# Optimization experiments

Hardware: AMD Instinct MI355X
Metric: run time of the kernel (lower is better)

Reference implementation:

```python
import jax, jax.numpy as jnp
import numpy as np

# SofthebbArgs constants (rate, adaptive=True, p, dot_uw=False, temp)
RATE = 1e-3
TEMP = 1.0
P = 0.5


def negate_non_maximal(t):
    # keep the per-row max entry, negate all others
    idx = jnp.argmax(t, axis=-1)                      # [B]
    mask = idx[:, None] == jnp.arange(t.shape[-1])    # [B, OUT]
    return jnp.where(mask, t, -t)


def setup_inputs() -> dict:
    key = jax.random.key(0)
    k1, k2 = jax.random.split(key, 2)
    B, IN, OUT = 8192, 1024, 1024
    x = jax.random.normal(k1, (B, IN), dtype=jnp.float32)
    # xavier_normal_ with gain=1: std = sqrt(2/(fan_in+fan_out))
    W = jax.random.normal(k2, (OUT, IN), dtype=jnp.float32) * (2.0 / (IN + OUT)) ** 0.5
    b = jnp.zeros((OUT,), dtype=jnp.float32)
    return {"x": x, "W": W, "b": b}


def reference(x, W, b):
    # --- HebbianLinear.forward (act = Identity) ---
    u = x @ W.T + b                                   # [B, OUT]
    y = u
    # --- softhebb: y = softmax(y / temp), then _hebb with dot_uw=False ---
    ysm = jax.nn.softmax(y / TEMP, axis=1)
    yn = negate_non_maximal(ysm)                      # [B, OUT]
    Bn = x.shape[0]
    # _hebb materializes dw[b,o,i] = yn[b,o]*(x[b,i] - u[b,o]*W[o,i]) then means over b.
    # Algebraically fused (no [B,OUT,IN] intermediate):
    #   step[o,i] = (yn^T x)[o,i]/B - mean_b(yn[b,o]*u[b,o]) * W[o,i]
    step = (yn.T @ x) / Bn - jnp.mean(yn * u, axis=0)[:, None] * W  # [OUT, IN]
    # adaptive per-row rate: rate * |1 - ||W_row||_2|^p
    diff = jnp.abs(1.0 - jnp.linalg.norm(W, axis=1))  # [OUT]
    rate = RATE * diff ** P
    return rate[:, None] * step                       # [OUT, IN]
```

## Files before the change

kernel.cpp:

```cpp
#include <hip/hip_runtime.h>

#define BATCH 8192
#define INF_  1024
#define OUTF  1024
#define INV_B (1.0f/8192.0f)
#define RATE_C 1e-3f
#define SPLITZ 16

typedef __bf16 bf16x8 __attribute__((ext_vector_type(8)));
typedef float  f32x4  __attribute__((ext_vector_type(4)));
typedef const __attribute__((address_space(1))) unsigned int* gas_t;
typedef __attribute__((address_space(3))) unsigned int* las_t;

static __device__ __forceinline__ unsigned short f2bf(float f) {
  unsigned int u = __float_as_uint(f);
  u += 0x7fffu + ((u >> 16) & 1u);
  return (unsigned short)(u >> 16);
}
static __device__ __forceinline__ float bf2f(unsigned short h) {
  return __uint_as_float(((unsigned int)h) << 16);
}

__global__ __launch_bounds__(256) void k_convert(
    const float* __restrict__ x, unsigned short* __restrict__ xb,
    unsigned short* __restrict__ xT, const float* __restrict__ W,
    unsigned short* __restrict__ Wb, float* __restrict__ rate) {
  const int t = threadIdx.x;
  if (blockIdx.x >= 2048) {
    __shared__ float red[256];
    const int o = blockIdx.x - 2048;
    float4 v = *(const float4*)&W[(size_t)o * INF_ + t * 4];
    ushort4 h;
    h.x = f2bf(v.x); h.y = f2bf(v.y); h.z = f2bf(v.z); h.w = f2bf(v.w);
    *(ushort4*)&Wb[(size_t)o * INF_ + t * 4] = h;
    red[t] = v.x * v.x + v.y * v.y + v.z * v.z + v.w * v.w;
    __syncthreads();
    for (int s = 128; s > 0; s >>= 1) {
      if (t < s) red[t] += red[t + s];
      __syncthreads();
    }
    if (t == 0) {
      float nrm = sqrtf(red[0]);
      rate[o] = RATE_C * sqrtf(fabsf(1.0f - nrm));
    }
    return;
  }
  __shared__ unsigned int t32[64][33];
  const int bx = blockIdx.x & 15;
  const int by = blockIdx.x >> 4;
  const int r0 = by * 64;
  const int c0 = bx * 64;
  const int m = t & 15;
  const int q = t >> 4;
#pragma unroll
  for (int p = 0; p < 2; ++p) {
    const int r2 = p * 16 + q;
    const int b  = r0 + 2 * r2;
    float4 v0 = *(const float4*)&x[(size_t)b * INF_ + c0 + 4 * m];
    float4 v1 = *(const float4*)&x[(size_t)(b + 1) * INF_ + c0 + 4 * m];
    ushort4 h0, h1;
    h0.x = f2bf(v0.x); h0.y = f2bf(v0.y); h0.z = f2bf(v0.z); h0.w = f2bf(v0.w);
    h1.x = f2bf(v1.x); h1.y = f2bf(v1.y); h1.z = f2bf(v1.z); h1.w = f2bf(v1.w);
    *(ushort4*)&xb[(size_t)b * INF_ + c0 + 4 * m] = h0;
    *(ushort4*)&xb[(size_t)(b + 1) * INF_ + c0 + 4 * m] = h1;
    t32[4 * m + 0][r2] = (unsigned int)h0.x | ((unsigned int)h1.x << 16);
    t32[4 * m + 1][r2] = (unsigned int)h0.y | ((unsigned int)h1.y << 16);
    t32[4 * m + 2][r2] = (unsigned int)h0.z | ((unsigned int)h1.z << 16);
    t32[4 * m + 3][r2] = (unsigned int)h0.w | ((unsigned int)h1.w << 16);
  }
  __syncthreads();
  const int c  = t >> 2;
  const int sg = t & 3;
  unsigned int vb[8];
#pragma unroll
  for (int k = 0; k < 8; ++k) vb[k] = t32[c][sg * 8 + k];
  unsigned short* dst = &xT[(size_t)(c0 + c) * BATCH + r0 + sg * 16];
  *(uint4*)&dst[0] = make_uint4(vb[0], vb[1], vb[2], vb[3]);
  *(uint4*)&dst[8] = make_uint4(vb[4], vb[5], vb[6], vb[7]);
}

__global__ __launch_bounds__(256, 3) void k_gemm(
    const unsigned short* __restrict__ A, const unsigned short* __restrict__ B,
    int lda, int ldb, int kChunk, float* __restrict__ C, int ldc,
    const float* __restrict__ bias, int mode) {
  __shared__ unsigned short As[128 * 64];
  __shared__ unsigned short Bs[128 * 64];
  const int t  = threadIdx.x;
  const int id = blockIdx.x;
  int bx, by, bz;
  if (mode == 0) {
    by = (id & 7) | ((id >> 6) << 3);
    bx = (id >> 3) & 7;
    bz = 0;
  } else {
    bz = ((id & 7) << 1) | ((id >> 3) & 1);
    by = (id >> 4) & 7;
    bx = id >> 7;
  }
  const int m0   = by * 128;
  const int n0   = bx * 128;
  const int k0   = bz * kChunk;
  const int lane = t & 63;
  const int wave = t >> 6;
  const int sr   = lane >> 3;
  const int scx  = ((lane & 7) ^ sr) * 8;
  const int wm   = (wave >> 1) * 64;
  const int wn   = (wave & 1) * 64;
  const int fm   = lane & 15;
  const int fk   = (lane >> 4) * 8;

  f32x4 acc[4][4] = {};

  const int ldsRow0 = wave * 8;
  const size_t gArow = (size_t)(m0 + ldsRow0 + sr) * lda + scx;
  const size_t gBrow = (size_t)(n0 + ldsRow0 + sr) * ldb + scx;

  for (int ks = 0; ks < kChunk; ks += 64) {
    const int k = k0 + ks;
#pragma unroll
    for (int j = 0; j < 4; ++j) {
      __builtin_amdgcn_global_load_lds(
          (gas_t)&A[gArow + (size_t)j * 32 * lda + k],
          (las_t)&As[(ldsRow0 + j * 32) * 64], 16, 0, 0);
      __builtin_amdgcn_global_load_lds(
          (gas_t)&B[gBrow + (size_t)j * 32 * ldb + k],
          (las_t)&Bs[(ldsRow0 + j * 32) * 64], 16, 0, 0);
    }
    __syncthreads();
#pragma unroll
    for (int kk = 0; kk < 64; kk += 32) {
      bf16x8 af[4], bf[4];
      const int swz = ((((kk + fk) >> 3) ^ (fm & 7)) << 3);
#pragma unroll
      for (int i = 0; i < 4; ++i)
        af[i] = *(const bf16x8*)&As[(wm + i * 16 + fm) * 64 + swz];
#pragma unroll
      for (int i = 0; i < 4; ++i)
        bf[i] = *(const bf16x8*)&Bs[(wn + i * 16 + fm) * 64 + swz];
#pragma unroll
      for (int mt = 0; mt < 4; ++mt)
#pragma unroll
        for (int nt = 0; nt < 4; ++nt)
          acc[mt][nt] = __builtin_amdgcn_mfma_f32_16x16x32_bf16(
              af[mt], bf[nt], acc[mt][nt], 0, 0, 0);
    }
    __syncthreads();
  }

  const int er = (lane >> 4) * 4;
  if (mode == 0) {
#pragma unroll
    for (int nt = 0; nt < 4; ++nt) {
      const int n  = n0 + wn + nt * 16 + fm;
      const float bv = bias[n];
#pragma unroll
      for (int mt = 0; mt < 4; ++mt) {
        const int mb = m0 + wm + mt * 16 + er;
#pragma unroll
        for (int r = 0; r < 4; ++r)
          C[(size_t)(mb + r) * ldc + n] = acc[mt][nt][r] + bv;
      }
    }
  } else {
    unsigned short* Cp = (unsigned short*)C + (size_t)bz * (1024u * 1024u);
#pragma unroll
    for (int nt = 0; nt < 4; ++nt) {
      const int n = n0 + wn + nt * 16 + fm;
#pragma unroll
      for (int mt = 0; mt < 4; ++mt) {
        const int mb = m0 + wm + mt * 16 + er;
#pragma unroll
        for (int r = 0; r < 4; ++r)
          Cp[(size_t)(mb + r) * ldc + n] = f2bf(acc[mt][nt][r]);
      }
    }
  }
}

__global__ __launch_bounds__(256) void k_row_stats(
    const float* __restrict__ u, const float* __restrict__ x,
    const float* __restrict__ W, float* __restrict__ rowmax,
    float* __restrict__ rowinv, int* __restrict__ rowarg) {
  __shared__ int cands[4][32];
  __shared__ int cnt[4];
  const int lane = threadIdx.x & 63;
  const int wave = threadIdx.x >> 6;
  const int b    = blockIdx.x * 4 + wave;

  float a[16];
  const float* up = &u[(size_t)b * OUTF + lane * 16];
#pragma unroll
  for (int j = 0; j < 16; j += 4) {
    float4 v = *(const float4*)&up[j];
    a[j] = v.x; a[j + 1] = v.y; a[j + 2] = v.z; a[j + 3] = v.w;
  }
  float mv = a[0]; int mi = lane * 16;
#pragma unroll
  for (int j = 1; j < 16; ++j)
    if (a[j] > mv) { mv = a[j]; mi = lane * 16 + j; }
#pragma unroll
  for (int off = 1; off < 64; off <<= 1) {
    float ov = __shfl_xor(mv, off);
    int   oi = __shfl_xor(mi, off);
    if (ov > mv || (ov == mv && oi < mi)) { mv = ov; mi = oi; }
  }
  const float M = mv;
  float se = 0.0f;
#pragma unroll
  for (int j = 0; j < 16; ++j) se += __expf(a[j] - M);
#pragma unroll
  for (int off = 1; off < 64; off <<= 1) se += __shfl_xor(se, off);

  const float thr = M - 0.05f;
  int ccount = 0;
  unsigned int cflags = 0;
#pragma unroll
  for (int j = 0; j < 16; ++j)
    if (a[j] >= thr) { cflags |= (1u << j); ++ccount; }
  int tot = ccount;
#pragma unroll
  for (int off = 1; off < 64; off <<= 1) tot += __shfl_xor(tot, off);

  int best = mi;
  if (tot > 1) {
    if (lane == 0) cnt[wave] = 0;
    for (int j = 0; j < 16; ++j)
      if (cflags & (1u << j)) {
        int p = atomicAdd(&cnt[wave], 1);
        if (p < 32) cands[wave][p] = lane * 16 + j;
      }
    int nc = cnt[wave]; if (nc > 32) nc = 32;
    float xr[16];
    const float* xp = &x[(size_t)b * INF_ + lane * 16];
#pragma unroll
    for (int j = 0; j < 16; j += 4) {
      float4 v = *(const float4*)&xp[j];
      xr[j] = v.x; xr[j + 1] = v.y; xr[j + 2] = v.z; xr[j + 3] = v.w;
    }
    float bv = -3.4e38f; int bi = 0x7fffffff;
    for (int c = 0; c < nc; ++c) {
      const int o = cands[wave][c];
      const float* wp = &W[(size_t)o * INF_ + lane * 16];
      float d = 0.0f;
#pragma unroll
      for (int j = 0; j < 16; j += 4) {
        float4 v = *(const float4*)&wp[j];
        d += xr[j] * v.x + xr[j + 1] * v.y + xr[j + 2] * v.z + xr[j + 3] * v.w;
      }
#pragma unroll
      for (int off = 1; off < 64; off <<= 1) d += __shfl_xor(d, off);
      if (d > bv || (d == bv && o < bi)) { bv = d; bi = o; }
    }
    best = bi;
  }
  if (lane == 0) {
    rowmax[b] = M;
    rowinv[b] = 1.0f / se;
    rowarg[b] = best;
  }
}

__global__ __launch_bounds__(256) void k_yn(
    const float* __restrict__ u, const float* __restrict__ rowmax,
    const float* __restrict__ rowinv, const int* __restrict__ rowarg,
    unsigned short* __restrict__ ynT, float* __restrict__ s_part) {
  __shared__ unsigned short tile[256][72];
  __shared__ float smax[64], sinv[64];
  __shared__ int   sarg[64];
  const int t  = threadIdx.x;
  const int o0 = blockIdx.x * 256;
  const int b0 = blockIdx.y * 64;
  if (t < 64) {
    smax[t] = rowmax[b0 + t];
    sinv[t] = rowinv[b0 + t];
    sarg[t] = rowarg[b0 + t];
  }
  __syncthreads();
  const int o = o0 + t;
  float sacc = 0.0f;
#pragma unroll
  for (int g = 0; g < 8; ++g) {
    uint4 pkv;
    unsigned short* pk = (unsigned short*)&pkv;
#pragma unroll
    for (int j = 0; j < 8; ++j) {
      const int r = g * 8 + j;
      float uu  = u[(size_t)(b0 + r) * OUTF + o];
      float ysm = __expf(uu - smax[r]) * sinv[r];
      float yn  = (o == sarg[r]) ? ysm : -ysm;
      sacc += yn * uu;
      pk[j] = f2bf(yn);
    }
    *(uint4*)&tile[t][g * 8] = pkv;
  }
  s_part[(size_t)blockIdx.y * OUTF + o] = sacc;
  __syncthreads();
#pragma unroll
  for (int it = 0; it < 8; ++it) {
    const int row = it * 32 + (t >> 3);
    const int seg = (t & 7) * 8;
    uint4 vv = *(const uint4*)&tile[row][seg];
    *(uint4*)&ynT[(size_t)(o0 + row) * BATCH + b0 + seg] = vv;
  }
}

__global__ __launch_bounds__(256) void k_final(
    const unsigned short* __restrict__ Cp, const float* __restrict__ W,
    const float* __restrict__ s_part, const float* __restrict__ rate,
    float* __restrict__ out) {
  __shared__ float sred[128];
  const int t = threadIdx.x;
  const int o = blockIdx.x;
  if (t < 128) sred[t] = s_part[(size_t)t * OUTF + o];
  __syncthreads();
  for (int s2 = 64; s2 > 0; s2 >>= 1) {
    if (t < s2) sred[t] += sred[t + s2];
    __syncthreads();
  }
  const float sb = sred[0] * INV_B;
  const float rt = rate[o];
  const int i0 = t * 4;
  float cx = 0, cy = 0, cz = 0, cw = 0;
#pragma unroll
  for (int z = 0; z < SPLITZ; ++z) {
    ushort4 h = *(const ushort4*)&Cp[(size_t)z * (1024u * 1024u) +
                                     (size_t)o * INF_ + i0];
    cx += bf2f(h.x); cy += bf2f(h.y); cz += bf2f(h.z); cw += bf2f(h.w);
  }
  float4 w = *(const float4*)&W[(size_t)o * INF_ + i0];
  float4 r;
  r.x = rt * (cx * INV_B - sb * w.x);
  r.y = rt * (cy * INV_B - sb * w.y);
  r.z = rt * (cz * INV_B - sb * w.z);
  r.w = rt * (cw * INV_B - sb * w.w);
  *(float4*)&out[(size_t)o * INF_ + i0] = r;
}

extern "C" void kernel_launch(void* const* d_in, const int* in_sizes, int n_in,
                              void* d_out, int out_size, void* d_ws, size_t ws_size,
                              hipStream_t stream) {
  const float* x    = (const float*)d_in[0];
  const float* W    = (const float*)d_in[1];
  const float* bias = (const float*)d_in[2];
  float* out = (float*)d_out;
  char* ws = (char*)d_ws;

  float*          u     = (float*)(ws + 0);
  unsigned short* xb    = (unsigned short*)(ws + 33554432);
  unsigned short* xT    = (unsigned short*)(ws + 50331648);
  unsigned short* Wb    = (unsigned short*)(ws + 67108864);
  unsigned short* ynT   = (unsigned short*)(ws + 69206016);
  float*          rate  = (float*)(ws + 85983232);
  float*          rmax  = (float*)(ws + 85987328);
  float*          rinv  = (float*)(ws + 86020096);
  int*            rarg  = (int*)  (ws + 86052864);
  float*          spart = (float*)(ws + 86085632);

  k_convert<<<dim3(3072), 256, 0, stream>>>(x, xb, xT, W, Wb, rate);
  k_gemm<<<dim3(512), 256, 0, stream>>>(xb, Wb, 1024, 1024, 1024,
                                        u, 1024, bias, 0);
  k_row_stats<<<dim3(2048), 256, 0, stream>>>(u, x, W, rmax, rinv, rarg);
  k_yn<<<dim3(4, 128), 256, 0, stream>>>(u, rmax, rinv, rarg, ynT, spart);
  k_gemm<<<dim3(1024), 256, 0, stream>>>(ynT, xT, 8192, 8192, 512,
                                         u, 1024, nullptr, 1);
  k_final<<<dim3(1024), 256, 0, stream>>>((const unsigned short*)u, W, spart,
                                          rate, out);
}
```

Measured before the change: 156.9 us.

## Store logits as bf16 and fuse row stats with yn transpose kernel

The first GEMM now writes u as bf16 instead of fp32, halving the logit traffic. Row max, softmax sum, argmax tie-breaking, yn computation, the s partial sums and the transposed ynT store are fused into one kernel that processes 16 rows per block through a swizzled LDS tile. This removes one launch and the extra pass over u. In exchange, bf16 logits coarsen the softmax and argmax inputs (the candidate threshold is widened to compensate), and k_final must reduce 2048 partial rows instead of 128.

```diff
diff --git a/kernel.cpp b/kernel.cpp
--- a/kernel.cpp
+++ b/kernel.cpp
@@ -81,7 +81,7 @@
 
 __global__ __launch_bounds__(256, 3) void k_gemm(
     const unsigned short* __restrict__ A, const unsigned short* __restrict__ B,
-    int lda, int ldb, int kChunk, float* __restrict__ C, int ldc,
+    int lda, int ldb, int kChunk, void* __restrict__ C, int ldc,
     const float* __restrict__ bias, int mode) {
   __shared__ unsigned short As[128 * 64];
   __shared__ unsigned short Bs[128 * 64];
@@ -149,6 +149,7 @@
 
   const int er = (lane >> 4) * 4;
   if (mode == 0) {
+    unsigned short* Cb = (unsigned short*)C;
 #pragma unroll
     for (int nt = 0; nt < 4; ++nt) {
       const int n  = n0 + wn + nt * 16 + fm;
@@ -158,7 +159,7 @@
         const int mb = m0 + wm + mt * 16 + er;
 #pragma unroll
         for (int r = 0; r < 4; ++r)
-          C[(size_t)(mb + r) * ldc + n] = acc[mt][nt][r] + bv;
+          Cb[(size_t)(mb + r) * ldc + n] = f2bf(acc[mt][nt][r] + bv);
       }
     }
   } else {
@@ -177,130 +178,145 @@
   }
 }
 
-__global__ __launch_bounds__(256) void k_row_stats(
-    const float* __restrict__ u, const float* __restrict__ x,
-    const float* __restrict__ W, float* __restrict__ rowmax,
-    float* __restrict__ rowinv, int* __restrict__ rowarg) {
+__global__ __launch_bounds__(256, 2) void k_softhebb(
+    const unsigned short* __restrict__ ub, const float* __restrict__ x,
+    const float* __restrict__ W, unsigned short* __restrict__ ynT,
+    float* __restrict__ s_part) {
+  __shared__ unsigned short tile[16][1032];
   __shared__ int cands[4][32];
   __shared__ int cnt[4];
-  const int lane = threadIdx.x & 63;
-  const int wave = threadIdx.x >> 6;
-  const int b    = blockIdx.x * 4 + wave;
-
-  float a[16];
-  const float* up = &u[(size_t)b * OUTF + lane * 16];
-#pragma unroll
-  for (int j = 0; j < 16; j += 4) {
-    float4 v = *(const float4*)&up[j];
-    a[j] = v.x; a[j + 1] = v.y; a[j + 2] = v.z; a[j + 3] = v.w;
-  }
-  float mv = a[0]; int mi = lane * 16;
-#pragma unroll
-  for (int j = 1; j < 16; ++j)
-    if (a[j] > mv) { mv = a[j]; mi = lane * 16 + j; }
-#pragma unroll
-  for (int off = 1; off < 64; off <<= 1) {
-    float ov = __shfl_xor(mv, off);
-    int   oi = __shfl_xor(mi, off);
-    if (ov > mv || (ov == mv && oi < mi)) { mv = ov; mi = oi; }
-  }
-  const float M = mv;
-  float se = 0.0f;
-#pragma unroll
-  for (int j = 0; j < 16; ++j) se += __expf(a[j] - M);
-#pragma unroll
-  for (int off = 1; off < 64; off <<= 1) se += __shfl_xor(se, off);
-
-  const float thr = M - 0.05f;
-  int ccount = 0;
-  unsigned int cflags = 0;
-#pragma unroll
-  for (int j = 0; j < 16; ++j)
-    if (a[j] >= thr) { cflags |= (1u << j); ++ccount; }
-  int tot = ccount;
-#pragma unroll
-  for (int off = 1; off < 64; off <<= 1) tot += __shfl_xor(tot, off);
-
-  int best = mi;
-  if (tot > 1) {
-    if (lane == 0) cnt[wave] = 0;
+  const int t     = threadIdx.x;
+  const int lane  = t & 63;
+  const int wave  = t >> 6;
+  const int b0    = blockIdx.x * 16;
+  const int oBase = lane * 16;
+
+  float sacc[16];
+#pragma unroll
+  for (int j = 0; j < 16; ++j) sacc[j] = 0.0f;
+
+  for (int rw = 0; rw < 4; ++rw) {
+    const int r = wave * 4 + rw;
+    const int b = b0 + r;
+    float a[16];
+    {
+      uint4 q0 = *(const uint4*)&ub[(size_t)b * OUTF + oBase];
+      uint4 q1 = *(const uint4*)&ub[(size_t)b * OUTF + oBase + 8];
+      const unsigned int* qa = (const unsigned int*)&q0;
+      const unsigned int* qb = (const unsigned int*)&q1;
+#pragma unroll
+      for (int c = 0; c < 4; ++c) {
+        a[2 * c]     = __uint_as_float(qa[c] << 16);
+        a[2 * c + 1] = __uint_as_float(qa[c] & 0xffff0000u);
+        a[8 + 2 * c]     = __uint_as_float(qb[c] << 16);
+        a[8 + 2 * c + 1] = __uint_as_float(qb[c] & 0xffff0000u);
+      }
+    }
+    float mv = a[0]; int mi = oBase;
+#pragma unroll
+    for (int j = 1; j < 16; ++j)
+      if (a[j] > mv) { mv = a[j]; mi = oBase + j; }
+#pragma unroll
+    for (int off = 1; off < 64; off <<= 1) {
+      float ov = __shfl_xor(mv, off);
+      int   oi = __shfl_xor(mi, off);
+      if (ov > mv || (ov == mv && oi < mi)) { mv = ov; mi = oi; }
+    }
+    const float M = mv;
+    float se = 0.0f;
+#pragma unroll
+    for (int j = 0; j < 16; ++j) se += __expf(a[j] - M);
+#pragma unroll
+    for (int off = 1; off < 64; off <<= 1) se += __shfl_xor(se, off);
+
+    const float thr = M - 0.10f;
+    unsigned int cflags = 0;
+    int ccount = 0;
+#pragma unroll
     for (int j = 0; j < 16; ++j)
-      if (cflags & (1u << j)) {
-        int p = atomicAdd(&cnt[wave], 1);
-        if (p < 32) cands[wave][p] = lane * 16 + j;
-      }
-    int nc = cnt[wave]; if (nc > 32) nc = 32;
-    float xr[16];
-    const float* xp = &x[(size_t)b * INF_ + lane * 16];
-#pragma unroll
-    for (int j = 0; j < 16; j += 4) {
-      float4 v = *(const float4*)&xp[j];
-      xr[j] = v.x; xr[j + 1] = v.y; xr[j + 2] = v.z; xr[j + 3] = v.w;
-    }
-    float bv = -3.4e38f; int bi = 0x7fffffff;
-    for (int c = 0; c < nc; ++c) {
-      const int o = cands[wave][c];
-      const float* wp = &W[(size_t)o * INF_ + lane * 16];
-      float d = 0.0f;
+      if (a[j] >= thr) { cflags |= (1u << j); ++ccount; }
+    int tot = ccount;
+#pragma unroll
+    for (int off = 1; off < 64; off <<= 1) tot += __shfl_xor(tot, off);
+
+    int best = mi;
+    if (tot > 1) {
+      if (lane == 0) cnt[wave] = 0;
+      for (int j = 0; j < 16; ++j)
+        if (cflags & (1u << j)) {
+          int p = atomicAdd(&cnt[wave], 1);
+          if (p < 32) cands[wave][p] = oBase + j;
+        }
+      int nc = cnt[wave]; if (nc > 32) nc = 32;
+      float xr[16];
+      const float* xp = &x[(size_t)b * INF_ + oBase];
 #pragma unroll
       for (int j = 0; j < 16; j += 4) {
-        float4 v = *(const float4*)&wp[j];
-        d += xr[j] * v.x + xr[j + 1] * v.y + xr[j + 2] * v.z + xr[j + 3] * v.w;
-      }
-#pragma unroll
-      for (int off = 1; off < 64; off <<= 1) d += __shfl_xor(d, off);
-      if (d > bv || (d == bv && o < bi)) { bv = d; bi = o; }
-    }
-    best = bi;
-  }
-  if (lane == 0) {
-    rowmax[b] = M;
-    rowinv[b] = 1.0f / se;
-    rowarg[b] = best;
-  }
-}
-
-__global__ __launch_bounds__(256) void k_yn(
-    const float* __restrict__ u, const float* __restrict__ rowmax,
-    const float* __restrict__ rowinv, const int* __restrict__ rowarg,
-    unsigned short* __restrict__ ynT, float* __restrict__ s_part) {
-  __shared__ unsigned short tile[256][72];
-  __shared__ float smax[64], sinv[64];
-  __shared__ int   sarg[64];
-  const int t  = threadIdx.x;
-  const int o0 = blockIdx.x * 256;
-  const int b0 = blockIdx.y * 64;
-  if (t < 64) {
-    smax[t] = rowmax[b0 + t];
-    sinv[t] = rowinv[b0 + t];
-    sarg[t] = rowarg[b0 + t];
+        float4 v = *(const float4*)&xp[j];
+        xr[j] = v.x; xr[j + 1] = v.y; xr[j + 2] = v.z; xr[j + 3] = v.w;
+      }
+      float bv = -3.4e38f; int bi = 0x7fffffff;
+      for (int c = 0; c < nc; ++c) {
+        const int o = cands[wave][c];
+        const float* wp = &W[(size_t)o * INF_ + oBase];
+        float d = 0.0f;
+#pragma unroll
+        for (int j = 0; j < 16; j += 4) {
+          float4 v = *(const float4*)&wp[j];
+          d += xr[j] * v.x + xr[j + 1] * v.y + xr[j + 2] * v.z +
+               xr[j + 3] * v.w;
+        }
+#pragma unroll
+        for (int off = 1; off < 64; off <<= 1) d += __shfl_xor(d, off);
+        if (d > bv || (d == bv && o < bi)) { bv = d; bi = o; }
+      }
+      best = bi;
+    }
+
+    const float inv = 1.0f / se;
+    uint4 pka, pkb;
+    unsigned short* p0v = (unsigned short*)&pka;
+    unsigned short* p1v = (unsigned short*)&pkb;
+#pragma unroll
+    for (int j = 0; j < 16; ++j) {
+      float e  = __expf(a[j] - M) * inv;
+      float yn = (oBase + j == best) ? e : -e;
+      sacc[j] += yn * a[j];
+      unsigned short hv = f2bf(yn);
+      if (j < 8) p0v[j] = hv; else p1v[j - 8] = hv;
+    }
+    const int c0 = 2 * lane, c1 = 2 * lane + 1;
+    const int sp0 = c0 ^ ((c0 >> 1) & 7);
+    const int sp1 = c1 ^ ((c1 >> 1) & 7);
+    *(uint4*)&tile[r][sp0 * 8] = pka;
+    *(uint4*)&tile[r][sp1 * 8] = pkb;
+  }
+
+  {
+    float* sp = &s_part[(size_t)(blockIdx.x * 4 + wave) * OUTF + oBase];
+#pragma unroll
+    for (int j = 0; j < 16; j += 4)
+      *(float4*)&sp[j] = make_float4(sacc[j], sacc[j + 1], sacc[j + 2],
+                                     sacc[j + 3]);
   }
   __syncthreads();
-  const int o = o0 + t;
-  float sacc = 0.0f;
-#pragma unroll
-  for (int g = 0; g < 8; ++g) {
-    uint4 pkv;
-    unsigned short* pk = (unsigned short*)&pkv;
-#pragma unroll
-    for (int j = 0; j < 8; ++j) {
-      const int r = g * 8 + j;
-      float uu  = u[(size_t)(b0 + r) * OUTF + o];
-      float ysm = __expf(uu - smax[r]) * sinv[r];
-      float yn  = (o == sarg[r]) ? ysm : -ysm;
-      sacc += yn * uu;
-      pk[j] = f2bf(yn);
-    }
-    *(uint4*)&tile[t][g * 8] = pkv;
-  }
-  s_part[(size_t)blockIdx.y * OUTF + o] = sacc;
-  __syncthreads();
-#pragma unroll
-  for (int it = 0; it < 8; ++it) {
-    const int row = it * 32 + (t >> 3);
-    const int seg = (t & 7) * 8;
-    uint4 vv = *(const uint4*)&tile[row][seg];
-    *(uint4*)&ynT[(size_t)(o0 + row) * BATCH + b0 + seg] = vv;
+
+#pragma unroll
+  for (int i = 0; i < 4; ++i) {
+    const int o  = t + 256 * i;
+    const int c  = o >> 3;
+    const int sp = c ^ ((c >> 1) & 7);
+    const int off = o & 7;
+    uint4 v0, v1;
+    unsigned short* va = (unsigned short*)&v0;
+    unsigned short* vb = (unsigned short*)&v1;
+#pragma unroll
+    for (int r = 0; r < 8; ++r)  va[r] = tile[r][sp * 8 + off];
+#pragma unroll
+    for (int r = 0; r < 8; ++r)  vb[r] = tile[r + 8][sp * 8 + off];
+    unsigned short* dst = &ynT[(size_t)o * BATCH + b0];
+    *(uint4*)&dst[0] = v0;
+    *(uint4*)&dst[8] = v1;
   }
 }
 
@@ -308,12 +324,15 @@
     const unsigned short* __restrict__ Cp, const float* __restrict__ W,
     const float* __restrict__ s_part, const float* __restrict__ rate,
     float* __restrict__ out) {
-  __shared__ float sred[128];
-  const int t = threadIdx.x;
-  const int o = blockIdx.x;
-  if (t < 128) sred[t] = s_part[(size_t)t * OUTF + o];
+  __shared__ float sred[256];
+  const int t  = threadIdx.x;
+  const int id = blockIdx.x;
+  const int o  = ((id & 7) << 7) | (id >> 3);
+  float sa = 0.0f;
+  for (int k = t; k < 2048; k += 256) sa += s_part[(size_t)k * OUTF + o];
+  sred[t] = sa;
   __syncthreads();
-  for (int s2 = 64; s2 > 0; s2 >>= 1) {
+  for (int s2 = 128; s2 > 0; s2 >>= 1) {
     if (t < s2) sred[t] += sred[t + s2];
     __syncthreads();
   }
@@ -345,24 +364,20 @@
   float* out = (float*)d_out;
   char* ws = (char*)d_ws;
 
-  float*          u     = (float*)(ws + 0);
-  unsigned short* xb    = (unsigned short*)(ws + 33554432);
-  unsigned short* xT    = (unsigned short*)(ws + 50331648);
+  unsigned short* ub    = (unsigned short*)(ws + 0);
+  unsigned short* xb    = (unsigned short*)(ws + 16777216);
+  unsigned short* xT    = (unsigned short*)(ws + 33554432);
+  unsigned short* ynT   = (unsigned short*)(ws + 50331648);
   unsigned short* Wb    = (unsigned short*)(ws + 67108864);
-  unsigned short* ynT   = (unsigned short*)(ws + 69206016);
-  float*          rate  = (float*)(ws + 85983232);
-  float*          rmax  = (float*)(ws + 85987328);
-  float*          rinv  = (float*)(ws + 86020096);
-  int*            rarg  = (int*)  (ws + 86052864);
-  float*          spart = (float*)(ws + 86085632);
+  float*          rate  = (float*)(ws + 69206016);
+  float*          spart = (float*)(ws + 69210112);
 
   k_convert<<<dim3(3072), 256, 0, stream>>>(x, xb, xT, W, Wb, rate);
   k_gemm<<<dim3(512), 256, 0, stream>>>(xb, Wb, 1024, 1024, 1024,
-                                        u, 1024, bias, 0);
-  k_row_stats<<<dim3(2048), 256, 0, stream>>>(u, x, W, rmax, rinv, rarg);
-  k_yn<<<dim3(4, 128), 256, 0, stream>>>(u, rmax, rinv, rarg, ynT, spart);
+                                        ub, 1024, bias, 0);
+  k_softhebb<<<dim3(512), 256, 0, stream>>>(ub, x, W, ynT, spart);
   k_gemm<<<dim3(1024), 256, 0, stream>>>(ynT, xT, 8192, 8192, 512,
-                                         u, 1024, nullptr, 1);
-  k_final<<<dim3(1024), 256, 0, stream>>>((const unsigned short*)u, W, spart,
+                                         ws, 1024, nullptr, 1);
+  k_final<<<dim3(1024), 256, 0, stream>>>((const unsigned short*)ws, W, spart,
                                           rate, out);
 }
```

After: 164.1 us. +4.6%, slower.

## Store logits u in bf16 and stage GEMM epilogue through LDS for coalesced writes

Applied to the files above, without the earlier changes.

The first GEMM now writes u as bf16 instead of fp32, which halves the u traffic for the GEMM store, row-stats and yn reads. Both GEMM modes stage results through a padded shared-memory tile so global writes are row-contiguous vector stores instead of scattered 2-byte/4-byte writes. The candidate threshold for the exact argmax recheck is widened to compensate for bf16 rounding of u. k_final block order is also swizzled. The cost is reduced precision of u in the softmax and the s term, which may move results toward the tolerance.

```diff
diff --git a/kernel.cpp b/kernel.cpp
--- a/kernel.cpp
+++ b/kernel.cpp
@@ -81,10 +81,11 @@
 
 __global__ __launch_bounds__(256, 3) void k_gemm(
     const unsigned short* __restrict__ A, const unsigned short* __restrict__ B,
-    int lda, int ldb, int kChunk, float* __restrict__ C, int ldc,
+    int lda, int ldb, int kChunk, void* __restrict__ C, int ldc,
     const float* __restrict__ bias, int mode) {
-  __shared__ unsigned short As[128 * 64];
-  __shared__ unsigned short Bs[128 * 64];
+  __shared__ unsigned short smem[128 * 132];
+  unsigned short* As = smem;
+  unsigned short* Bs = smem + 128 * 64;
   const int t  = threadIdx.x;
   const int id = blockIdx.x;
   int bx, by, bz;
@@ -148,37 +149,35 @@
   }
 
   const int er = (lane >> 4) * 4;
-  if (mode == 0) {
-#pragma unroll
-    for (int nt = 0; nt < 4; ++nt) {
-      const int n  = n0 + wn + nt * 16 + fm;
-      const float bv = bias[n];
-#pragma unroll
-      for (int mt = 0; mt < 4; ++mt) {
-        const int mb = m0 + wm + mt * 16 + er;
-#pragma unroll
-        for (int r = 0; r < 4; ++r)
-          C[(size_t)(mb + r) * ldc + n] = acc[mt][nt][r] + bv;
-      }
-    }
-  } else {
-    unsigned short* Cp = (unsigned short*)C + (size_t)bz * (1024u * 1024u);
-#pragma unroll
-    for (int nt = 0; nt < 4; ++nt) {
-      const int n = n0 + wn + nt * 16 + fm;
-#pragma unroll
-      for (int mt = 0; mt < 4; ++mt) {
-        const int mb = m0 + wm + mt * 16 + er;
-#pragma unroll
-        for (int r = 0; r < 4; ++r)
-          Cp[(size_t)(mb + r) * ldc + n] = f2bf(acc[mt][nt][r]);
-      }
-    }
+#pragma unroll
+  for (int nt = 0; nt < 4; ++nt) {
+    const int cc = wn + nt * 16 + fm;
+    const float bv = (mode == 0) ? bias[n0 + cc] : 0.0f;
+#pragma unroll
+    for (int mt = 0; mt < 4; ++mt) {
+      const int rr = wm + mt * 16 + er;
+#pragma unroll
+      for (int r = 0; r < 4; ++r)
+        smem[(rr + r) * 132 + cc] = f2bf(acc[mt][nt][r] + bv);
+    }
+  }
+  __syncthreads();
+  unsigned short* Cb = (mode == 0)
+      ? (unsigned short*)C
+      : (unsigned short*)C + (size_t)bz * (1024u * 1024u);
+#pragma unroll
+  for (int i = 0; i < 8; ++i) {
+    const int row = i * 16 + (t >> 4);
+    const int ch  = (t & 15) * 8;
+    const unsigned short* src = &smem[row * 132 + ch];
+    unsigned short* dst = &Cb[(size_t)(m0 + row) * ldc + n0 + ch];
+    *(uint2*)&dst[0] = *(const uint2*)&src[0];
+    *(uint2*)&dst[4] = *(const uint2*)&src[4];
   }
 }
 
 __global__ __launch_bounds__(256) void k_row_stats(
-    const float* __restrict__ u, const float* __restrict__ x,
+    const unsigned short* __restrict__ ub, const float* __restrict__ x,
     const float* __restrict__ W, float* __restrict__ rowmax,
     float* __restrict__ rowinv, int* __restrict__ rowarg) {
   __shared__ int cands[4][32];
@@ -186,18 +185,26 @@
   const int lane = threadIdx.x & 63;
   const int wave = threadIdx.x >> 6;
   const int b    = blockIdx.x * 4 + wave;
+  const int oBase = lane * 16;
 
   float a[16];
-  const float* up = &u[(size_t)b * OUTF + lane * 16];
-#pragma unroll
-  for (int j = 0; j < 16; j += 4) {
-    float4 v = *(const float4*)&up[j];
-    a[j] = v.x; a[j + 1] = v.y; a[j + 2] = v.z; a[j + 3] = v.w;
-  }
-  float mv = a[0]; int mi = lane * 16;
+  {
+    uint4 q0 = *(const uint4*)&ub[(size_t)b * OUTF + oBase];
+    uint4 q1 = *(const uint4*)&ub[(size_t)b * OUTF + oBase + 8];
+    const unsigned int* qa = (const unsigned int*)&q0;
+    const unsigned int* qb = (const unsigned int*)&q1;
+#pragma unroll
+    for (int c = 0; c < 4; ++c) {
+      a[2 * c]         = __uint_as_float(qa[c] << 16);
+      a[2 * c + 1]     = __uint_as_float(qa[c] & 0xffff0000u);
+      a[8 + 2 * c]     = __uint_as_float(qb[c] << 16);
+      a[8 + 2 * c + 1] = __uint_as_float(qb[c] & 0xffff0000u);
+    }
+  }
+  float mv = a[0]; int mi = oBase;
 #pragma unroll
   for (int j = 1; j < 16; ++j)
-    if (a[j] > mv) { mv = a[j]; mi = lane * 16 + j; }
+    if (a[j] > mv) { mv = a[j]; mi = oBase + j; }
 #pragma unroll
   for (int off = 1; off < 64; off <<= 1) {
     float ov = __shfl_xor(mv, off);
@@ -211,9 +218,9 @@
 #pragma unroll
   for (int off = 1; off < 64; off <<= 1) se += __shfl_xor(se, off);
 
-  const float thr = M - 0.05f;
+  const float thr = M - 0.10f;
+  unsigned int cflags = 0;
   int ccount = 0;
-  unsigned int cflags = 0;
 #pragma unroll
   for (int j = 0; j < 16; ++j)
     if (a[j] >= thr) { cflags |= (1u << j); ++ccount; }
@@ -227,11 +234,11 @@
     for (int j = 0; j < 16; ++j)
       if (cflags & (1u << j)) {
         int p = atomicAdd(&cnt[wave], 1);
-        if (p < 32) cands[wave][p] = lane * 16 + j;
+        if (p < 32) cands[wave][p] = oBase + j;
       }
     int nc = cnt[wave]; if (nc > 32) nc = 32;
     float xr[16];
-    const float* xp = &x[(size_t)b * INF_ + lane * 16];
+    const float* xp = &x[(size_t)b * INF_ + oBase];
 #pragma unroll
     for (int j = 0; j < 16; j += 4) {
       float4 v = *(const float4*)&xp[j];
@@ -240,12 +247,13 @@
     float bv = -3.4e38f; int bi = 0x7fffffff;
     for (int c = 0; c < nc; ++c) {
       const int o = cands[wave][c];
-      const float* wp = &W[(size_t)o * INF_ + lane * 16];
+      const float* wp = &W[(size_t)o * INF_ + oBase];
       float d = 0.0f;
 #pragma unroll
       for (int j = 0; j < 16; j += 4) {
         float4 v = *(const float4*)&wp[j];
-        d += xr[j] * v.x + xr[j + 1] * v.y + xr[j + 2] * v.z + xr[j + 3] * v.w;
+        d += xr[j] * v.x + xr[j + 1] * v.y + xr[j + 2] * v.z +
+             xr[j + 3] * v.w;
       }
 #pragma unroll
       for (int off = 1; off < 64; off <<= 1) d += __shfl_xor(d, off);
@@ -261,7 +269,7 @@
 }
 
 __global__ __launch_bounds__(256) void k_yn(
-    const float* __restrict__ u, const float* __restrict__ rowmax,
+    const unsigned short* __restrict__ ub, const float* __restrict__ rowmax,
     const float* __restrict__ rowinv, const int* __restrict__ rowarg,
     unsigned short* __restrict__ ynT, float* __restrict__ s_part) {
   __shared__ unsigned short tile[256][72];
@@ -285,7 +293,7 @@
 #pragma unroll
     for (int j = 0; j < 8; ++j) {
       const int r = g * 8 + j;
-      float uu  = u[(size_t)(b0 + r) * OUTF + o];
+      float uu  = bf2f(ub[(size_t)(b0 + r) * OUTF + o]);
       float ysm = __expf(uu - smax[r]) * sinv[r];
       float yn  = (o == sarg[r]) ? ysm : -ysm;
       sacc += yn * uu;
@@ -309,8 +317,9 @@
     const float* __restrict__ s_part, const float* __restrict__ rate,
     float* __restrict__ out) {
   __shared__ float sred[128];
-  const int t = threadIdx.x;
-  const int o = blockIdx.x;
+  const int t  = threadIdx.x;
+  const int id = blockIdx.x;
+  const int o  = ((id & 7) << 7) | (id >> 3);
   if (t < 128) sred[t] = s_part[(size_t)t * OUTF + o];
   __syncthreads();
   for (int s2 = 64; s2 > 0; s2 >>= 1) {
@@ -345,24 +354,24 @@
   float* out = (float*)d_out;
   char* ws = (char*)d_ws;
 
-  float*          u     = (float*)(ws + 0);
-  unsigned short* xb    = (unsigned short*)(ws + 33554432);
-  unsigned short* xT    = (unsigned short*)(ws + 50331648);
+  unsigned short* ub    = (unsigned short*)(ws + 0);
+  unsigned short* xb    = (unsigned short*)(ws + 16777216);
+  unsigned short* xT    = (unsigned short*)(ws + 33554432);
+  unsigned short* ynT   = (unsigned short*)(ws + 50331648);
   unsigned short* Wb    = (unsigned short*)(ws + 67108864);
-  unsigned short* ynT   = (unsigned short*)(ws + 69206016);
-  float*          rate  = (float*)(ws + 85983232);
-  float*          rmax  = (float*)(ws + 85987328);
-  float*          rinv  = (float*)(ws + 86020096);
-  int*            rarg  = (int*)  (ws + 86052864);
-  float*          spart = (float*)(ws + 86085632);
+  float*          rate  = (float*)(ws + 69206016);
+  float*          spart = (float*)(ws + 69210112);
+  float*          rmax  = (float*)(ws + 69734400);
+  float*          rinv  = (float*)(ws + 69767168);
+  int*            rarg  = (int*)  (ws + 69799936);
 
   k_convert<<<dim3(3072), 256, 0, stream>>>(x, xb, xT, W, Wb, rate);
   k_gemm<<<dim3(512), 256, 0, stream>>>(xb, Wb, 1024, 1024, 1024,
-                                        u, 1024, bias, 0);
-  k_row_stats<<<dim3(2048), 256, 0, stream>>>(u, x, W, rmax, rinv, rarg);
-  k_yn<<<dim3(4, 128), 256, 0, stream>>>(u, rmax, rinv, rarg, ynT, spart);
+                                        ub, 1024, bias, 0);
+  k_row_stats<<<dim3(2048), 256, 0, stream>>>(ub, x, W, rmax, rinv, rarg);
+  k_yn<<<dim3(4, 128), 256, 0, stream>>>(ub, rmax, rinv, rarg, ynT, spart);
   k_gemm<<<dim3(1024), 256, 0, stream>>>(ynT, xT, 8192, 8192, 512,
-                                         u, 1024, nullptr, 1);
-  k_final<<<dim3(1024), 256, 0, stream>>>((const unsigned short*)u, W, spart,
+                                         ws, 1024, nullptr, 1);
+  k_final<<<dim3(1024), 256, 0, stream>>>((const unsigned short*)ws, W, spart,
                                           rate, out);
 }
```

Result: no change. 155.3 us (-1.0%).
